# Kernel tuning notes

Measured on AMD Instinct MI355X. Metric: run time of the kernel, lower is better.

Reference implementation:

```python
import jax, jax.numpy as jnp
import numpy as np

N, D = 100000, 128
S = [25, 10]


def setup_inputs() -> dict:
    key = jax.random.key(0)
    ks = jax.random.split(key, 5)
    scale = 1.0 / np.sqrt(2 * D)  # keep sigmoid out of saturation
    Z = jax.random.normal(ks[0], (N, D), dtype=jnp.float32)
    W0 = jax.random.normal(ks[1], (2 * D, D), dtype=jnp.float32) * scale
    b0 = jnp.zeros((D,), dtype=jnp.float32)
    W1 = jax.random.normal(ks[2], (2 * D, D), dtype=jnp.float32) * scale
    b1 = jnp.zeros((D,), dtype=jnp.float32)
    neigh0 = jax.random.randint(ks[3], (N, S[0]), 0, N, dtype=jnp.int32)
    neigh1 = jax.random.randint(ks[4], (N, S[1]), 0, N, dtype=jnp.int32)
    return {"Z": Z, "W0": W0, "b0": b0, "W1": W1, "b1": b1,
            "neigh0": neigh0, "neigh1": neigh1}


def _sage_layer(Z, W, b, neigh):
    # Z: [N, D]; neigh: [N, s] int indices into rows of Z
    zn = jnp.mean(Z[neigh], axis=1)                     # gather + mean-aggregate: [N, D]
    h = jax.nn.sigmoid(jnp.concatenate([Z, zn], axis=-1) @ W + b)  # [N, D]
    return h / jnp.linalg.norm(h, axis=-1, keepdims=True)          # L2 normalize


def reference(Z, W0, b0, W1, b1, neigh0, neigh1):
    Z = _sage_layer(Z, W0, b0, neigh0)  # layer k=0, s=25
    Z = _sage_layer(Z, W1, b1, neigh1)  # layer k=1, s=10
    return Z
```

## Files before the change

### kernel.cpp

```cpp
#include <hip/hip_runtime.h>

typedef unsigned short u16;
typedef unsigned int   u32;
typedef __attribute__((ext_vector_type(8))) short short8;
typedef __attribute__((ext_vector_type(4))) float f32x4;

#define D 128
#define SWZ(idx, r) ((idx) ^ (((r) & 7) << 3))

__device__ __forceinline__ u16 f2bf(float x) {
    union { float f; u32 u; } v; v.f = x;
    u32 r = v.u + 0x7fffu + ((v.u >> 16) & 1u);
    return (u16)(r >> 16);
}

__global__ __launch_bounds__(256) void convert_z(
    const float4* __restrict__ Z4, ushort4* __restrict__ Zb4, int n4)
{
    int i = blockIdx.x * 256 + threadIdx.x;
    if (i < n4) {
        float4 v = Z4[i];
        ushort4 u; u.x = f2bf(v.x); u.y = f2bf(v.y); u.z = f2bf(v.z); u.w = f2bf(v.w);
        Zb4[i] = u;
    }
}

__global__ __launch_bounds__(256) void transpose_w(
    const float* __restrict__ W, u16* __restrict__ WT)
{
    int t = blockIdx.x * 256 + threadIdx.x;
    if (t < 256 * 128) {
        int k = t >> 7, j = t & 127;
        WT[j * 256 + k] = f2bf(W[t]);
    }
}

template<int S>
__global__ __launch_bounds__(256) void sage_gather_b(
    const u16* __restrict__ T, int tstride, const int* __restrict__ neigh,
    u16* __restrict__ XA, int N)
{
    int wid = (int)((blockIdx.x * 256 + threadIdx.x) >> 6);
    wid = __builtin_amdgcn_readfirstlane(wid);
    const int lane = threadIdx.x & 63;
    if (wid >= N) return;
    const int* nb = neigh + (size_t)wid * S;
    float ax = 0.f, ay = 0.f;
#pragma unroll
    for (int j = 0; j < S; ++j) {
        const int r = nb[j];
        const u32 v = *(const u32*)(T + (size_t)r * tstride + lane * 2);
        union { u32 u; float f; } lo, hi;
        lo.u = v << 16; hi.u = v & 0xffff0000u;
        ax += lo.f; ay += hi.f;
    }
    const float inv = 1.0f / (float)S;
    const u32 packed = ((u32)f2bf(ay * inv) << 16) | (u32)f2bf(ax * inv);
    *(u32*)(XA + (size_t)wid * D + lane * 2) = packed;
}

template<int MODE>
__global__ __launch_bounds__(256) void sage_gemm_mfma(
    const void* __restrict__ Xs_, const u16* __restrict__ Xa,
    const u16* __restrict__ WTg, const float* __restrict__ bias,
    void* __restrict__ out_, int N)
{
    __shared__ __align__(16) u16 XT[128 * 256];
    __shared__ __align__(16) u16 WT[128 * 256];

    const int t = threadIdx.x;
    const int block0 = blockIdx.x * 128;

    if (MODE == 0) {
        const float* Xs = (const float*)Xs_;
#pragma unroll
        for (int i = 0; i < 16; ++i) {
            int c = t + i * 256, r = c >> 5, f4 = c & 31, gn = block0 + r;
            float4 v = make_float4(0.f, 0.f, 0.f, 0.f);
            if (gn < N) v = *(const float4*)(Xs + (size_t)gn * D + f4 * 4);
            ushort4 u; u.x = f2bf(v.x); u.y = f2bf(v.y); u.z = f2bf(v.z); u.w = f2bf(v.w);
            *(ushort4*)&XT[SWZ(r * 256 + f4 * 4, r)] = u;
        }
    } else {
        const u16* Xs = (const u16*)Xs_;
#pragma unroll
        for (int i = 0; i < 8; ++i) {
            int c = t + i * 256, r = c >> 4, o = c & 15, gn = block0 + r;
            uint4 v = make_uint4(0u, 0u, 0u, 0u);
            if (gn < N) v = *(const uint4*)(Xs + (size_t)gn * 256 + o * 8);
            *(uint4*)&XT[SWZ(r * 256 + o * 8, r)] = v;
        }
    }
#pragma unroll
    for (int i = 0; i < 8; ++i) {
        int c = t + i * 256, r = c >> 4, o = c & 15, gn = block0 + r;
        uint4 v = make_uint4(0u, 0u, 0u, 0u);
        if (gn < N) v = *(const uint4*)(Xa + (size_t)gn * D + o * 8);
        *(uint4*)&XT[SWZ(r * 256 + 128 + o * 8, r)] = v;
    }
#pragma unroll
    for (int i = 0; i < 16; ++i) {
        int c = t + i * 256, r = c >> 5, o = c & 31;
        uint4 v = *(const uint4*)(WTg + r * 256 + o * 8);
        *(uint4*)&WT[SWZ(r * 256 + o * 8, r)] = v;
    }
    __syncthreads();

    const int w = t >> 6, l = t & 63;
    const int l15 = l & 15, lq = l >> 4;
    f32x4 acc[2][8];
#pragma unroll
    for (int m = 0; m < 2; ++m)
#pragma unroll
        for (int n = 0; n < 8; ++n) acc[m][n] = (f32x4){0.f, 0.f, 0.f, 0.f};

#pragma unroll
    for (int ks = 0; ks < 8; ++ks) {
        const int ak = ks * 32 + lq * 8;
        const int r0 = w * 32 + l15, r1 = w * 32 + 16 + l15;
        short8 a0 = *(const short8*)&XT[SWZ(r0 * 256 + ak, r0)];
        short8 a1 = *(const short8*)&XT[SWZ(r1 * 256 + ak, r1)];
#pragma unroll
        for (int nf = 0; nf < 8; ++nf) {
            const int jr = nf * 16 + l15;
            short8 b = *(const short8*)&WT[SWZ(jr * 256 + ak, jr)];
            acc[0][nf] = __builtin_amdgcn_mfma_f32_16x16x32_bf16(a0, b, acc[0][nf], 0, 0, 0);
            acc[1][nf] = __builtin_amdgcn_mfma_f32_16x16x32_bf16(a1, b, acc[1][nf], 0, 0, 0);
        }
    }

    float bs[8];
#pragma unroll
    for (int nf = 0; nf < 8; ++nf) bs[nf] = bias[nf * 16 + l15];

    __syncthreads();
#pragma unroll
    for (int mf = 0; mf < 2; ++mf) {
#pragma unroll
        for (int rg = 0; rg < 4; ++rg) {
            const int r = w * 32 + mf * 16 + lq * 4 + rg;
            float h[8]; float ss = 0.f;
#pragma unroll
            for (int nf = 0; nf < 8; ++nf) {
                const float a = acc[mf][nf][rg] + bs[nf];
                h[nf] = 1.0f / (1.0f + __expf(-a));
                ss += h[nf] * h[nf];
            }
            ss += __shfl_xor(ss, 1); ss += __shfl_xor(ss, 2);
            ss += __shfl_xor(ss, 4); ss += __shfl_xor(ss, 8);
            const float inv = rsqrtf(ss);
            if (MODE == 0) {
#pragma unroll
                for (int nf = 0; nf < 8; ++nf)
                    XT[r * 128 + nf * 16 + l15] = f2bf(h[nf] * inv);
            } else {
                float* OL = (float*)XT;
#pragma unroll
                for (int nf = 0; nf < 8; ++nf)
                    OL[r * 128 + nf * 16 + l15] = h[nf] * inv;
            }
        }
    }
    __syncthreads();

    if (MODE == 0) {
        u16* Hb = (u16*)out_;
#pragma unroll
        for (int i = 0; i < 8; ++i) {
            int c = t + i * 256, r = c >> 4, o = c & 15, gn = block0 + r;
            if (gn < N)
                *(uint4*)(Hb + (size_t)gn * 256 + o * 8) = *(const uint4*)&XT[r * 128 + o * 8];
        }
    } else {
        float* O = (float*)out_;
        const float* OL = (const float*)XT;
#pragma unroll
        for (int i = 0; i < 16; ++i) {
            int c = t + i * 256, r = c >> 5, o = c & 31, gn = block0 + r;
            if (gn < N)
                *(float4*)(O + (size_t)gn * D + o * 4) = *(const float4*)&OL[r * 128 + o * 4];
        }
    }
}

extern "C" void kernel_launch(void* const* d_in, const int* in_sizes, int n_in,
                              void* d_out, int out_size, void* d_ws, size_t ws_size,
                              hipStream_t stream) {
    const float* Z  = (const float*)d_in[0];
    const float* W0 = (const float*)d_in[1];
    const float* b0 = (const float*)d_in[2];
    const float* W1 = (const float*)d_in[3];
    const float* b1 = (const float*)d_in[4];
    const int*   n0 = (const int*)d_in[5];
    const int*   n1 = (const int*)d_in[6];
    const int N = in_sizes[0] / D;

    const size_t zbBytes = (size_t)N * D * 2;
    u16* Zb  = (u16*)d_ws;
    u16* XA0 = (u16*)((char*)d_ws + zbBytes);
    u16* W1T = (u16*)d_ws;
    u16* W0T = (u16*)((char*)d_ws + 65536);
    u16* XA1 = (u16*)((char*)d_ws + 131072);
    u16* Hb  = (u16*)d_out;
    float* out = (float*)d_out;

    const int n4 = (N * D) / 4;
    const int cvtBlocks    = (n4 + 255) / 256;
    const int gatherBlocks = (N + 3) / 4;
    const int gemmBlocks   = (N + 127) / 128;

    convert_z<<<cvtBlocks, 256, 0, stream>>>((const float4*)Z, (ushort4*)Zb, n4);
    sage_gather_b<25><<<gatherBlocks, 256, 0, stream>>>(Zb, 128, n0, XA0, N);
    transpose_w<<<128, 256, 0, stream>>>(W1, W1T);
    transpose_w<<<128, 256, 0, stream>>>(W0, W0T);
    sage_gemm_mfma<0><<<gemmBlocks, 256, 0, stream>>>((const void*)Z, XA0, W0T, b0, (void*)Hb, N);
    sage_gather_b<10><<<gatherBlocks, 256, 0, stream>>>(Hb, 256, n1, XA1, N);
    sage_gemm_mfma<1><<<gemmBlocks, 256, 0, stream>>>((const void*)Hb, XA1, W1T, b1, (void*)out, N);
}
```

Baseline: 337.3 us.

## Load GEMM activations into registers, drop X LDS tile and fuse W transpose

The GEMM kernel now reads its X rows (bf16 Z or Hb plus the aggregated neighbours) straight from global memory into registers as MFMA B operands, and swaps operand roles so each wave computes a transposed tile. This removes the 64KB X shared-memory tile, which halves LDS use and may allow more blocks per CU. The separate transpose_w kernels are removed; every block now converts and transposes fp32 W into LDS itself, which repeats that work across roughly 800 blocks through strided global reads. The epilogue becomes a column-wise normalization with vector LDS stores using a new swizzle, and layer 0 reuses the bf16 Zb instead of reconverting fp32 Z.

```diff
diff --git a/kernel.cpp b/kernel.cpp
--- a/kernel.cpp
+++ b/kernel.cpp
@@ -6,7 +6,8 @@
 typedef __attribute__((ext_vector_type(4))) float f32x4;
 
 #define D 128
-#define SWZ(idx, r) ((idx) ^ (((r) & 7) << 3))
+#define SWZ(idx, r)  ((idx) ^ (((r) & 7) << 3))
+#define SWZF(idx, r) ((idx) ^ (((r) & 7) << 2))
 
 __device__ __forceinline__ u16 f2bf(float x) {
     union { float f; u32 u; } v; v.f = x;
@@ -22,16 +23,6 @@
         float4 v = Z4[i];
         ushort4 u; u.x = f2bf(v.x); u.y = f2bf(v.y); u.z = f2bf(v.z); u.w = f2bf(v.w);
         Zb4[i] = u;
-    }
-}
-
-__global__ __launch_bounds__(256) void transpose_w(
-    const float* __restrict__ W, u16* __restrict__ WT)
-{
-    int t = blockIdx.x * 256 + threadIdx.x;
-    if (t < 256 * 128) {
-        int k = t >> 7, j = t & 127;
-        WT[j * 256 + k] = f2bf(W[t]);
     }
 }
 
@@ -61,103 +52,114 @@
 
 template<int MODE>
 __global__ __launch_bounds__(256) void sage_gemm_mfma(
-    const void* __restrict__ Xs_, const u16* __restrict__ Xa,
-    const u16* __restrict__ WTg, const float* __restrict__ bias,
+    const u16* __restrict__ Xs, int xs_stride, const u16* __restrict__ Xa,
+    const float* __restrict__ W, const float* __restrict__ bias,
     void* __restrict__ out_, int N)
 {
-    __shared__ __align__(16) u16 XT[128 * 256];
     __shared__ __align__(16) u16 WT[128 * 256];
 
     const int t = threadIdx.x;
     const int block0 = blockIdx.x * 128;
-
-    if (MODE == 0) {
-        const float* Xs = (const float*)Xs_;
-#pragma unroll
-        for (int i = 0; i < 16; ++i) {
-            int c = t + i * 256, r = c >> 5, f4 = c & 31, gn = block0 + r;
-            float4 v = make_float4(0.f, 0.f, 0.f, 0.f);
-            if (gn < N) v = *(const float4*)(Xs + (size_t)gn * D + f4 * 4);
-            ushort4 u; u.x = f2bf(v.x); u.y = f2bf(v.y); u.z = f2bf(v.z); u.w = f2bf(v.w);
-            *(ushort4*)&XT[SWZ(r * 256 + f4 * 4, r)] = u;
-        }
-    } else {
-        const u16* Xs = (const u16*)Xs_;
-#pragma unroll
-        for (int i = 0; i < 8; ++i) {
-            int c = t + i * 256, r = c >> 4, o = c & 15, gn = block0 + r;
-            uint4 v = make_uint4(0u, 0u, 0u, 0u);
-            if (gn < N) v = *(const uint4*)(Xs + (size_t)gn * 256 + o * 8);
-            *(uint4*)&XT[SWZ(r * 256 + o * 8, r)] = v;
-        }
-    }
-#pragma unroll
-    for (int i = 0; i < 8; ++i) {
-        int c = t + i * 256, r = c >> 4, o = c & 15, gn = block0 + r;
-        uint4 v = make_uint4(0u, 0u, 0u, 0u);
-        if (gn < N) v = *(const uint4*)(Xa + (size_t)gn * D + o * 8);
-        *(uint4*)&XT[SWZ(r * 256 + 128 + o * 8, r)] = v;
-    }
-#pragma unroll
-    for (int i = 0; i < 16; ++i) {
-        int c = t + i * 256, r = c >> 5, o = c & 31;
-        uint4 v = *(const uint4*)(WTg + r * 256 + o * 8);
-        *(uint4*)&WT[SWZ(r * 256 + o * 8, r)] = v;
-    }
-    __syncthreads();
-
     const int w = t >> 6, l = t & 63;
     const int l15 = l & 15, lq = l >> 4;
+
+    const int row0 = min(block0 + w * 32 + l15,      N - 1);
+    const int row1 = min(block0 + w * 32 + 16 + l15, N - 1);
+
+    short8 b0[8];
+#pragma unroll
+    for (int ks = 0; ks < 8; ++ks) {
+        const int k0 = ks * 32 + lq * 8;
+        const u16* p = (ks < 4) ? (Xs + (size_t)row0 * xs_stride + k0)
+                                : (Xa + (size_t)row0 * 128 + (k0 - 128));
+        b0[ks] = *(const short8*)p;
+    }
+
+    {
+        const int j = t & 127, g = t >> 7;
+#pragma unroll
+        for (int kk = 0; kk < 64; ++kk) {
+            const int k = g * 128 + kk * 2;
+            const float wa = W[(size_t)k * 128 + j];
+            const float wb = W[(size_t)(k + 1) * 128 + j];
+            const u32 pk = ((u32)f2bf(wb) << 16) | (u32)f2bf(wa);
+            *(u32*)&WT[SWZ(j * 256 + k, j)] = pk;
+        }
+    }
+    __syncthreads();
+
     f32x4 acc[2][8];
 #pragma unroll
     for (int m = 0; m < 2; ++m)
 #pragma unroll
         for (int n = 0; n < 8; ++n) acc[m][n] = (f32x4){0.f, 0.f, 0.f, 0.f};
 
+    short8 b1[8];
+#pragma unroll
+    for (int ks = 0; ks < 8; ++ks) {
+        const int k0 = ks * 32 + lq * 8;
+        const u16* p = (ks < 4) ? (Xs + (size_t)row1 * xs_stride + k0)
+                                : (Xa + (size_t)row1 * 128 + (k0 - 128));
+        b1[ks] = *(const short8*)p;
+    }
+
 #pragma unroll
     for (int ks = 0; ks < 8; ++ks) {
         const int ak = ks * 32 + lq * 8;
-        const int r0 = w * 32 + l15, r1 = w * 32 + 16 + l15;
-        short8 a0 = *(const short8*)&XT[SWZ(r0 * 256 + ak, r0)];
-        short8 a1 = *(const short8*)&XT[SWZ(r1 * 256 + ak, r1)];
 #pragma unroll
         for (int nf = 0; nf < 8; ++nf) {
             const int jr = nf * 16 + l15;
-            short8 b = *(const short8*)&WT[SWZ(jr * 256 + ak, jr)];
-            acc[0][nf] = __builtin_amdgcn_mfma_f32_16x16x32_bf16(a0, b, acc[0][nf], 0, 0, 0);
-            acc[1][nf] = __builtin_amdgcn_mfma_f32_16x16x32_bf16(a1, b, acc[1][nf], 0, 0, 0);
-        }
-    }
-
-    float bs[8];
-#pragma unroll
-    for (int nf = 0; nf < 8; ++nf) bs[nf] = bias[nf * 16 + l15];
+            short8 a = *(const short8*)&WT[SWZ(jr * 256 + ak, jr)];
+            acc[0][nf] = __builtin_amdgcn_mfma_f32_16x16x32_bf16(a, b0[ks], acc[0][nf], 0, 0, 0);
+        }
+    }
+#pragma unroll
+    for (int ks = 0; ks < 8; ++ks) {
+        const int ak = ks * 32 + lq * 8;
+#pragma unroll
+        for (int nf = 0; nf < 8; ++nf) {
+            const int jr = nf * 16 + l15;
+            short8 a = *(const short8*)&WT[SWZ(jr * 256 + ak, jr)];
+            acc[1][nf] = __builtin_amdgcn_mfma_f32_16x16x32_bf16(a, b1[ks], acc[1][nf], 0, 0, 0);
+        }
+    }
+
+    float4 bs4[8];
+#pragma unroll
+    for (int nf = 0; nf < 8; ++nf)
+        bs4[nf] = *(const float4*)(bias + nf * 16 + lq * 4);
 
     __syncthreads();
+
 #pragma unroll
     for (int mf = 0; mf < 2; ++mf) {
-#pragma unroll
-        for (int rg = 0; rg < 4; ++rg) {
-            const int r = w * 32 + mf * 16 + lq * 4 + rg;
-            float h[8]; float ss = 0.f;
+        const int nloc = w * 32 + mf * 16 + l15;
+        float h[8][4]; float ss = 0.f;
+#pragma unroll
+        for (int nf = 0; nf < 8; ++nf)
+#pragma unroll
+            for (int rg = 0; rg < 4; ++rg) {
+                const float a = acc[mf][nf][rg] + bs4[nf][rg];
+                const float s = 1.0f / (1.0f + __expf(-a));
+                h[nf][rg] = s; ss += s * s;
+            }
+        ss += __shfl_xor(ss, 16); ss += __shfl_xor(ss, 32);
+        const float inv = rsqrtf(ss);
+        if (MODE == 0) {
 #pragma unroll
             for (int nf = 0; nf < 8; ++nf) {
-                const float a = acc[mf][nf][rg] + bs[nf];
-                h[nf] = 1.0f / (1.0f + __expf(-a));
-                ss += h[nf] * h[nf];
+                ushort4 o;
+                o.x = f2bf(h[nf][0] * inv); o.y = f2bf(h[nf][1] * inv);
+                o.z = f2bf(h[nf][2] * inv); o.w = f2bf(h[nf][3] * inv);
+                *(ushort4*)&WT[SWZ(nloc * 128 + nf * 16 + lq * 4, nloc)] = o;
             }
-            ss += __shfl_xor(ss, 1); ss += __shfl_xor(ss, 2);
-            ss += __shfl_xor(ss, 4); ss += __shfl_xor(ss, 8);
-            const float inv = rsqrtf(ss);
-            if (MODE == 0) {
-#pragma unroll
-                for (int nf = 0; nf < 8; ++nf)
-                    XT[r * 128 + nf * 16 + l15] = f2bf(h[nf] * inv);
-            } else {
-                float* OL = (float*)XT;
-#pragma unroll
-                for (int nf = 0; nf < 8; ++nf)
-                    OL[r * 128 + nf * 16 + l15] = h[nf] * inv;
+        } else {
+            float* OL = (float*)WT;
+#pragma unroll
+            for (int nf = 0; nf < 8; ++nf) {
+                float4 o = make_float4(h[nf][0]*inv, h[nf][1]*inv,
+                                       h[nf][2]*inv, h[nf][3]*inv);
+                *(float4*)&OL[SWZF(nloc * 128 + nf * 16 + lq * 4, nloc)] = o;
             }
         }
     }
@@ -169,16 +171,18 @@
         for (int i = 0; i < 8; ++i) {
             int c = t + i * 256, r = c >> 4, o = c & 15, gn = block0 + r;
             if (gn < N)
-                *(uint4*)(Hb + (size_t)gn * 256 + o * 8) = *(const uint4*)&XT[r * 128 + o * 8];
+                *(uint4*)(Hb + (size_t)gn * 256 + o * 8) =
+                    *(const uint4*)&WT[SWZ(r * 128 + o * 8, r)];
         }
     } else {
         float* O = (float*)out_;
-        const float* OL = (const float*)XT;
+        const float* OL = (const float*)WT;
 #pragma unroll
         for (int i = 0; i < 16; ++i) {
             int c = t + i * 256, r = c >> 5, o = c & 31, gn = block0 + r;
             if (gn < N)
-                *(float4*)(O + (size_t)gn * D + o * 4) = *(const float4*)&OL[r * 128 + o * 4];
+                *(float4*)(O + (size_t)gn * D + o * 4) =
+                    *(const float4*)&OL[SWZF(r * 128 + o * 4, r)];
         }
     }
 }
@@ -198,11 +202,8 @@
     const size_t zbBytes = (size_t)N * D * 2;
     u16* Zb  = (u16*)d_ws;
     u16* XA0 = (u16*)((char*)d_ws + zbBytes);
-    u16* W1T = (u16*)d_ws;
-    u16* W0T = (u16*)((char*)d_ws + 65536);
-    u16* XA1 = (u16*)((char*)d_ws + 131072);
+    u16* XA1 = (u16*)d_ws;
     u16* Hb  = (u16*)d_out;
-    float* out = (float*)d_out;
 
     const int n4 = (N * D) / 4;
     const int cvtBlocks    = (n4 + 255) / 256;
@@ -211,9 +212,7 @@
 
     convert_z<<<cvtBlocks, 256, 0, stream>>>((const float4*)Z, (ushort4*)Zb, n4);
     sage_gather_b<25><<<gatherBlocks, 256, 0, stream>>>(Zb, 128, n0, XA0, N);
-    transpose_w<<<128, 256, 0, stream>>>(W1, W1T);
-    transpose_w<<<128, 256, 0, stream>>>(W0, W0T);
-    sage_gemm_mfma<0><<<gemmBlocks, 256, 0, stream>>>((const void*)Z, XA0, W0T, b0, (void*)Hb, N);
+    sage_gemm_mfma<0><<<gemmBlocks, 256, 0, stream>>>(Zb, 128, XA0, W0, b0, (void*)Hb, N);
     sage_gather_b<10><<<gatherBlocks, 256, 0, stream>>>(Hb, 256, n1, XA1, N);
-    sage_gemm_mfma<1><<<gemmBlocks, 256, 0, stream>>>((const void*)Hb, XA1, W1T, b1, (void*)out, N);
-}
+    sage_gemm_mfma<1><<<gemmBlocks, 256, 0, stream>>>(Hb, 256, XA1, W1, b1, d_out, N);
+}
```

After: 317.1 us. -6.0%, faster.
